# Performance work log

Hardware: AMD Instinct MI355X
Metric: run time of the kernel (lower is better)

Reference implementation:

```python
import jax, jax.numpy as jnp
import numpy as np

E = 512   # decoder embedding dim
H = 2048  # decoder hidden size


def setup_inputs() -> dict:
    key = jax.random.key(0)
    ks = jax.random.split(key, 10)
    V, B, T, S = 50000, 32, 128, 128
    s = 0.05
    return {
        "embed_table": jax.random.normal(ks[0], (V, E), jnp.float32) * s,
        "encoder_outs": jax.random.normal(ks[1], (S, B, 2 * 512), jnp.float32),
        "encoder_hiddens": jax.random.normal(ks[2], (1, B, H), jnp.float32) * s,
        "encoder_cells": jax.random.normal(ks[3], (1, B, H), jnp.float32) * s,
        "W_ih": jax.random.normal(ks[4], (4 * H, 2048), jnp.float32) * s,
        "W_hh": jax.random.normal(ks[5], (4 * H, H), jnp.float32) * s,
        "b_ih": jax.random.normal(ks[6], (4 * H,), jnp.float32) * s,
        "b_hh": jax.random.normal(ks[7], (4 * H,), jnp.float32) * s,
        "prev_output_tokens": jax.random.randint(ks[8], (B, T), 0, V),
        "tgt_langs": jax.random.randint(ks[9], (B,), 0, V),
    }


def reference(embed_table, encoder_outs, encoder_hiddens, encoder_cells,
              W_ih, W_hh, b_ih, b_hh, prev_output_tokens, tgt_langs):
    # bottleneck: max-pool encoder states over source time (LASER-style)
    context = jnp.max(encoder_outs, axis=0)                 # [B, 2*enc_hidden]
    x = embed_table[prev_output_tokens]                      # [B, T, E]
    x = jnp.transpose(x, (1, 0, 2))                          # [T, B, E]
    lang_embed = embed_table[tgt_langs]                      # [B, E]

    # Per-step LSTM input is concat(x_t, lang, context). lang/context are
    # time-invariant, so precompute their gate contribution once.
    static_in = jnp.concatenate([lang_embed, context], axis=1)   # [B, E + 2*enc]
    gates_x = (jnp.einsum('tbe,ge->tbg', x, W_ih[:, :E])
               + static_in @ W_ih[:, E:].T + b_ih + b_hh)        # [T, B, 4H]

    h0 = encoder_hiddens[0]
    c0 = encoder_cells[0]

    def step(carry, g_x):
        h, c = carry
        gates = g_x + h @ W_hh.T                              # [B, 4H]
        i, f, g, o = jnp.split(gates, 4, axis=1)
        c = jax.nn.sigmoid(f) * c + jax.nn.sigmoid(i) * jnp.tanh(g)
        h = jax.nn.sigmoid(o) * jnp.tanh(c)
        return (h, c), h

    _, outs = jax.lax.scan(step, (h0, c0), gates_x)           # [T, B, H]
    return outs
```

## Files before the change

### kernel.cpp

```cpp
#include <hip/hip_runtime.h>
#include <math.h>

#define E_DIM 512
#define H_DIM 2048
#define G_DIM 8192
#define B_DIM 32
#define T_DIM 128
#define S_DIM 128
#define ENC2  1024
#define SI_DIM 1536

#define NBLK 256
#define NTHR 512
#define JT   8
#define KHW  (H_DIM/8)
#define KXW  (E_DIM/8)
#define HB   (B_DIM*H_DIM)
#define HPLANE 65536



typedef __bf16 bf16_t;
typedef bf16_t bf16x8 __attribute__((ext_vector_type(8)));
typedef float f32x4 __attribute__((ext_vector_type(4)));
typedef unsigned int u32x4 __attribute__((ext_vector_type(4)));

__device__ __forceinline__ unsigned short f2bf(float x) {
    unsigned u = __float_as_uint(x);
    u += 0x7FFFu + ((u >> 16) & 1u);
    return (unsigned short)(u >> 16);
}
__device__ __forceinline__ float bf2f(unsigned short s) {
    return __uint_as_float(((unsigned)s) << 16);
}
__device__ __forceinline__ unsigned pack2(float a, float b) {
    return (unsigned)f2bf(a) | ((unsigned)f2bf(b) << 16);
}
__device__ __forceinline__ f32x4 mfma16(bf16x8 a, bf16x8 b, f32x4 c) {
    return __builtin_amdgcn_mfma_f32_16x16x32_bf16(a, b, c, 0, 0, 0);
}
__device__ __forceinline__ bf16x8 tofrag(u32x4 q) {
    return __builtin_bit_cast(bf16x8, q);
}
__device__ __forceinline__ float sigf(float x) { return 1.f / (1.f + expf(-x)); }

#define OPAQUE(v) asm volatile("" : "+v"(v))
#define ALD(p) __hip_atomic_load((p), __ATOMIC_RELAXED, __HIP_MEMORY_SCOPE_AGENT)
#define AST(p, v) __hip_atomic_store((p), (v), __ATOMIC_RELAXED, __HIP_MEMORY_SCOPE_AGENT)

struct WPair { u32x4 hi, lo; };
__device__ __forceinline__ WPair packW(const float* src) {
    float4 w0 = *(const float4*)src;
    float4 w1 = *(const float4*)(src + 16);
    u32x4 qh;
    qh.x = pack2(w0.x, w0.y); qh.y = pack2(w0.z, w0.w);
    qh.z = pack2(w1.x, w1.y); qh.w = pack2(w1.z, w1.w);
    float r0 = w0.x - bf2f((unsigned short)(qh.x & 0xFFFF));
    float r1 = w0.y - bf2f((unsigned short)(qh.x >> 16));
    float r2 = w0.z - bf2f((unsigned short)(qh.y & 0xFFFF));
    float r3 = w0.w - bf2f((unsigned short)(qh.y >> 16));
    float r4 = w1.x - bf2f((unsigned short)(qh.z & 0xFFFF));
    float r5 = w1.y - bf2f((unsigned short)(qh.z >> 16));
    float r6 = w1.z - bf2f((unsigned short)(qh.w & 0xFFFF));
    float r7 = w1.w - bf2f((unsigned short)(qh.w >> 16));
    u32x4 ql;
    ql.x = pack2(r0, r1); ql.y = pack2(r2, r3);
    ql.z = pack2(r4, r5); ql.w = pack2(r6, r7);
    WPair out; out.hi = qh; out.lo = ql;
    return out;
}

__global__ void k_prep(const float* __restrict__ enc_outs, const float* __restrict__ embed,
                       const int* __restrict__ langs, const float* __restrict__ h0,
                       float* __restrict__ si, unsigned short* __restrict__ hth,
                       unsigned short* __restrict__ htl, unsigned int* __restrict__ flags) {
    int tid = blockIdx.x * blockDim.x + threadIdx.x;
    int np = gridDim.x * blockDim.x;
    for (int i = tid; i < NBLK * 16; i += np)
        flags[i] = 0u;
    for (int i = tid; i < B_DIM * ENC2; i += np) {
        int b = i >> 10, e = i & 1023;
        float m = -3.4e38f;
        for (int s = 0; s < S_DIM; ++s)
            m = fmaxf(m, enc_outs[(s * B_DIM + b) * ENC2 + e]);
        si[b * SI_DIM + E_DIM + e] = m;
    }
    for (int i = tid; i < B_DIM * E_DIM; i += np) {
        int b = i >> 9, e = i & 511;
        si[b * SI_DIM + e] = embed[(long)langs[b] * E_DIM + e];
    }
    for (int i = tid; i < B_DIM * H_DIM; i += np) {
        int b = i >> 11, j = i & 2047;
        float h = h0[i];
        unsigned short hi = f2bf(h);
        unsigned short lo = f2bf(h - bf2f(hi));
        int T = j >> 5, lgp = (j & 15) >> 2, o = (j & 3) + 4 * ((j & 31) >> 4);
        int idx = ((T * 4 + lgp) * 32 + b) * 8 + o;
        hth[idx] = hi;
        htl[idx] = lo;
    }
}

__global__ void k_gather_x(const float* __restrict__ embed, const int* __restrict__ tok,
                           unsigned short* __restrict__ xh, unsigned short* __restrict__ xl) {
    int r = blockIdx.x;
    int t = r >> 5, b = r & 31;
    long row = tok[b * T_DIM + t];
    const float4* src = (const float4*)(embed + row * E_DIM);
    unsigned* xhp = (unsigned*)(xh + (size_t)t * 16384);
    unsigned* xlp = (unsigned*)(xl + (size_t)t * 16384);
    for (int g = threadIdx.x; g < 128; g += blockDim.x) {
        float4 v = src[g];
        unsigned h01 = pack2(v.x, v.y), h23 = pack2(v.z, v.w);
        float rx = v.x - bf2f((unsigned short)(h01 & 0xFFFF));
        float ry = v.y - bf2f((unsigned short)(h01 >> 16));
        float rz = v.z - bf2f((unsigned short)(h23 & 0xFFFF));
        float rw = v.w - bf2f((unsigned short)(h23 >> 16));
        int T = g >> 3, lgp = g & 3, o0 = 4 * ((g & 7) >> 2);
        int u32i = ((T * 4 + lgp) * 32 + b) * 4 + (o0 >> 1);
        uint2 qh; qh.x = h01; qh.y = h23;
        uint2 ql; ql.x = pack2(rx, ry); ql.y = pack2(rz, rw);
        *(uint2*)(xhp + u32i) = qh;
        *(uint2*)(xlp + u32i) = ql;
    }
}

#define MFMA12(PH, PL, IT) \
    acc00 = mfma16(Ah0, tofrag(PH##0##IT), acc00); \
    acc00 = mfma16(Ah0, tofrag(PL##0##IT), acc00); \
    acc00 = mfma16(Al0, tofrag(PH##0##IT), acc00); \
    acc01 = mfma16(Ah1, tofrag(PH##0##IT), acc01); \
    acc01 = mfma16(Ah1, tofrag(PL##0##IT), acc01); \
    acc01 = mfma16(Al1, tofrag(PH##0##IT), acc01); \
    acc10 = mfma16(Ah0, tofrag(PH##1##IT), acc10); \
    acc10 = mfma16(Ah0, tofrag(PL##1##IT), acc10); \
    acc10 = mfma16(Al0, tofrag(PH##1##IT), acc10); \
    acc11 = mfma16(Ah1, tofrag(PH##1##IT), acc11); \
    acc11 = mfma16(Ah1, tofrag(PL##1##IT), acc11); \
    acc11 = mfma16(Al1, tofrag(PH##1##IT), acc11);

#define AX_IT(IT) do { \
    const int fb = ((wv * 2 + (IT)) * 4 + lg) * 32 + lr; \
    bf16x8 Ah0 = __builtin_bit_cast(bf16x8, xh4[fb]); \
    bf16x8 Ah1 = __builtin_bit_cast(bf16x8, xh4[fb + 16]); \
    bf16x8 Al0 = __builtin_bit_cast(bf16x8, xl4[fb]); \
    bf16x8 Al1 = __builtin_bit_cast(bf16x8, xl4[fb + 16]); \
    MFMA12(Xh, Xl, IT) \
} while (0)

#define AH_IT(IT) do { \
    const int fb = ((wv * 8 + (IT)) * 4 + lg) * 32 + lr; \
    bf16x8 Ah0 = __builtin_bit_cast(bf16x8, hh4[fb]); \
    bf16x8 Ah1 = __builtin_bit_cast(bf16x8, hh4[fb + 16]); \
    bf16x8 Al0 = __builtin_bit_cast(bf16x8, hl4[fb]); \
    bf16x8 Al1 = __builtin_bit_cast(bf16x8, hl4[fb + 16]); \
    MFMA12(Wh, Wl, IT) \
} while (0)

#define PK_HH(F, IT) { WPair p = packW(W_hh + (long)rowf##F * H_DIM + (wv * KHW + IT * 32 + 4 * lg)); \
                       Wh##F##IT = p.hi; Wl##F##IT = p.lo; }
#define PK_X(F, IT)  { WPair p = packW(W_ih + (long)rowf##F * 2048 + (wv * KXW + IT * 32 + 4 * lg)); \
                       Xh##F##IT = p.hi; Xl##F##IT = p.lo; }

__global__ __launch_bounds__(NTHR, 2) void k_lstm(
        const unsigned short* __restrict__ xh, const unsigned short* __restrict__ xl,
        unsigned short* __restrict__ hth, unsigned short* __restrict__ htl,
        const float* __restrict__ si, const float* __restrict__ W_ih,
        const float* __restrict__ W_hh, const float* __restrict__ b_ih,
        const float* __restrict__ b_hh, const float* __restrict__ c0,
        float* __restrict__ out, unsigned int* __restrict__ flags) {
    __shared__ f32x4 red[8][2][2][64];
    __shared__ float sgl[4][B_DIM][JT];

    const int tid = threadIdx.x;
    const int wv = tid >> 6, l = tid & 63, lr = l & 15, lg = l >> 4;
    const int jb = blockIdx.x * JT;

    {
        int c = tid >> 4, bp = tid & 15;
        int gate = c >> 3, jl = c & 7;
        long grow = (long)(gate * H_DIM + jb + jl);
        const float* wrow = W_ih + grow * 2048 + E_DIM;
        const float* s0 = si + bp * SI_DIM;
        const float* s1 = si + (bp + 16) * SI_DIM;
        float a0 = 0.f, a1 = 0.f;
        for (int k = 0; k < SI_DIM; k += 4) {
            float4 w  = *(const float4*)(wrow + k);
            float4 x0 = *(const float4*)(s0 + k);
            float4 x1 = *(const float4*)(s1 + k);
            a0 += w.x * x0.x + w.y * x0.y + w.z * x0.z + w.w * x0.w;
            a1 += w.x * x1.x + w.y * x1.y + w.z * x1.z + w.w * x1.w;
        }
        float bias = b_ih[grow] + b_hh[grow];
        sgl[gate][bp][jl] = a0 + bias;
        sgl[gate][bp + 16][jl] = a1 + bias;
    }

    const int rowf0 = ((lr >> 3)) * H_DIM + jb + (lr & 7);
    const int rowf1 = (2 + (lr >> 3)) * H_DIM + jb + (lr & 7);

    u32x4 Wh00, Wh01, Wh02, Wh03, Wh04, Wh05, Wh06, Wh07;
    u32x4 Wh10, Wh11, Wh12, Wh13, Wh14, Wh15, Wh16, Wh17;
    u32x4 Wl00, Wl01, Wl02, Wl03, Wl04, Wl05, Wl06, Wl07;
    u32x4 Wl10, Wl11, Wl12, Wl13, Wl14, Wl15, Wl16, Wl17;
    u32x4 Xh00, Xh01, Xh10, Xh11, Xl00, Xl01, Xl10, Xl11;

    PK_HH(0, 0) PK_HH(0, 1) PK_HH(0, 2) PK_HH(0, 3)
    PK_HH(0, 4) PK_HH(0, 5) PK_HH(0, 6) PK_HH(0, 7)
    PK_HH(1, 0) PK_HH(1, 1) PK_HH(1, 2) PK_HH(1, 3)
    PK_HH(1, 4) PK_HH(1, 5) PK_HH(1, 6) PK_HH(1, 7)
    PK_X(0, 0) PK_X(0, 1) PK_X(1, 0) PK_X(1, 1)

    OPAQUE(Wh00); OPAQUE(Wh01); OPAQUE(Wh02); OPAQUE(Wh03);
    OPAQUE(Wh04); OPAQUE(Wh05); OPAQUE(Wh06); OPAQUE(Wh07);
    OPAQUE(Wh10); OPAQUE(Wh11); OPAQUE(Wh12); OPAQUE(Wh13);
    OPAQUE(Wh14); OPAQUE(Wh15); OPAQUE(Wh16); OPAQUE(Wh17);
    OPAQUE(Wl00); OPAQUE(Wl01); OPAQUE(Wl02); OPAQUE(Wl03);
    OPAQUE(Wl04); OPAQUE(Wl05); OPAQUE(Wl06); OPAQUE(Wl07);
    OPAQUE(Wl10); OPAQUE(Wl11); OPAQUE(Wl12); OPAQUE(Wl13);
    OPAQUE(Wl14); OPAQUE(Wl15); OPAQUE(Wl16); OPAQUE(Wl17);
    OPAQUE(Xh00); OPAQUE(Xh01); OPAQUE(Xh10); OPAQUE(Xh11);
    OPAQUE(Xl00); OPAQUE(Xl01); OPAQUE(Xl10); OPAQUE(Xl11);

    const int ab = tid >> 3, ajl = tid & 7;
    float creg = 0.f;
    if (tid < 256) creg = c0[ab * H_DIM + jb + ajl];

    __syncthreads();

    #pragma unroll 1
    for (int t = 0; t < T_DIM; ++t) {
        f32x4 acc00 = {}, acc01 = {}, acc10 = {}, acc11 = {};

        {
            const uint4* xh4 = (const uint4*)(xh + (size_t)t * 16384);
            const uint4* xl4 = (const uint4*)(xl + (size_t)t * 16384);
            AX_IT(0); AX_IT(1);
        }

        if (t > 0) {
            const unsigned tgt = (unsigned)t;
            const bool mine = (l < 32);
            const unsigned int* fp = flags + (size_t)(wv * 32 + (l & 31)) * 16;
            for (;;) {
                unsigned v = mine ? ALD(fp) : tgt;
                if (__all(v >= tgt)) break;
                __builtin_amdgcn_s_sleep(1);
            }
            __builtin_amdgcn_sched_barrier(0);
        }

        {
            const uint4* hh4 = (const uint4*)(hth + (size_t)t * HPLANE);
            const uint4* hl4 = (const uint4*)(htl + (size_t)t * HPLANE);
            AH_IT(0); AH_IT(1); AH_IT(2); AH_IT(3);
            AH_IT(4); AH_IT(5); AH_IT(6); AH_IT(7);
        }

        red[wv][0][0][l] = acc00; red[wv][0][1][l] = acc01;
        red[wv][1][0][l] = acc10; red[wv][1][1][l] = acc11;
        __syncthreads();

        float hn = 0.f;
        if (tid < 256) {
            const int m = ab >> 4, r = ab & 3, q = (ab & 15) >> 2;
            float gs[4];
            #pragma unroll
            for (int g = 0; g < 4; ++g) {
                const int l2 = (q << 4) | ((g & 1) * 8 + ajl);
                float s = 0.f;
                #pragma unroll
                for (int w = 0; w < 8; ++w)
                    s += red[w][g >> 1][m][l2][r];
                gs[g] = s + sgl[g][ab][ajl];
            }
            float cn = sigf(gs[1]) * creg + sigf(gs[0]) * tanhf(gs[2]);
            hn = sigf(gs[3]) * tanhf(cn);
            creg = cn;
            unsigned short hh = f2bf(hn);
            unsigned short hl = f2bf(hn - bf2f(hh));
            unsigned nhh = __shfl_down((unsigned)hh, 1);
            unsigned nhl = __shfl_down((unsigned)hl, 1);
            if ((ajl & 1) == 0) {
                unsigned* hthn = (unsigned*)(hth + (size_t)(t + 1) * HPLANE);
                unsigned* htln = (unsigned*)(htl + (size_t)(t + 1) * HPLANE);
                int j0 = jb + ajl;
                int T = j0 >> 5, lgp = (j0 & 15) >> 2;
                int o = (j0 & 3) + 4 * ((j0 & 31) >> 4);
                int u32i = ((T * 4 + lgp) * 32 + ab) * 4 + (o >> 1);
                AST(hthn + u32i, (unsigned)hh | (nhh << 16));
                AST(htln + u32i, (unsigned)hl | (nhl << 16));
            }
        }

        asm volatile("s_waitcnt vmcnt(0)" ::: "memory");
        __syncthreads();
        if (tid == 0 && t < T_DIM - 1)
            AST(flags + (size_t)blockIdx.x * 16, (unsigned)(t + 1));

        if (tid < 256)
            out[(size_t)t * HB + ab * H_DIM + jb + ajl] = hn;
    }
}

extern "C" void kernel_launch(void* const* d_in, const int* in_sizes, int n_in,
                              void* d_out, int out_size, void* d_ws, size_t ws_size,
                              hipStream_t stream) {
    const float* embed    = (const float*)d_in[0];
    const float* enc_outs = (const float*)d_in[1];
    const float* h0       = (const float*)d_in[2];
    const float* c0       = (const float*)d_in[3];
    const float* W_ih     = (const float*)d_in[4];
    const float* W_hh     = (const float*)d_in[5];
    const float* b_ih     = (const float*)d_in[6];
    const float* b_hh     = (const float*)d_in[7];
    const int*   tok      = (const int*)d_in[8];
    const int*   langs    = (const int*)d_in[9];
    float* out = (float*)d_out;

    char* ws = (char*)d_ws;
    unsigned short* xh  = (unsigned short*)(ws + 0);
    unsigned short* xl  = (unsigned short*)(ws + 4194304);
    unsigned short* hth = (unsigned short*)(ws + 8388608);
    unsigned short* htl = (unsigned short*)(ws + 25296896);
    float*          si  = (float*)(ws + 42205184);
    unsigned int* flags = (unsigned int*)(ws + 42401792);

    hipLaunchKernelGGL(k_prep, dim3(512), dim3(256), 0, stream,
                       enc_outs, embed, langs, h0, si, hth, htl, flags);
    hipLaunchKernelGGL(k_gather_x, dim3(T_DIM * B_DIM), dim3(128), 0, stream,
                       embed, tok, xh, xl);
    hipLaunchKernelGGL(k_lstm, dim3(NBLK), dim3(NTHR), 0, stream,
                       xh, xl, hth, htl, si, W_ih, W_hh, b_ih, b_hh, c0,
                       out, flags);
}
```

Measured before the change: 981.4 us.

## Split LSTM step into two batch-half phases with separate sync flags

Each timestep is now processed as two half-batch phases (batches 0-15 then 16-31). Each phase has its own grid-wide flag slot, so one half's recurrent matmul can proceed while other blocks are still finishing the other half. The aim is to let the inter-block barrier latency of one half overlap with compute on the other half. In exchange there are twice as many barriers and flag waits per step, smaller MFMA batches per phase, and fewer active threads in the elementwise stage.

```diff
diff --git a/kernel.cpp b/kernel.cpp
--- a/kernel.cpp
+++ b/kernel.cpp
@@ -125,42 +125,97 @@
     }
 }
 
-#define MFMA12(PH, PL, IT) \
-    acc00 = mfma16(Ah0, tofrag(PH##0##IT), acc00); \
-    acc00 = mfma16(Ah0, tofrag(PL##0##IT), acc00); \
-    acc00 = mfma16(Al0, tofrag(PH##0##IT), acc00); \
-    acc01 = mfma16(Ah1, tofrag(PH##0##IT), acc01); \
-    acc01 = mfma16(Ah1, tofrag(PL##0##IT), acc01); \
-    acc01 = mfma16(Al1, tofrag(PH##0##IT), acc01); \
-    acc10 = mfma16(Ah0, tofrag(PH##1##IT), acc10); \
-    acc10 = mfma16(Ah0, tofrag(PL##1##IT), acc10); \
-    acc10 = mfma16(Al0, tofrag(PH##1##IT), acc10); \
-    acc11 = mfma16(Ah1, tofrag(PH##1##IT), acc11); \
-    acc11 = mfma16(Ah1, tofrag(PL##1##IT), acc11); \
-    acc11 = mfma16(Al1, tofrag(PH##1##IT), acc11);
-
-#define AX_IT(IT) do { \
-    const int fb = ((wv * 2 + (IT)) * 4 + lg) * 32 + lr; \
-    bf16x8 Ah0 = __builtin_bit_cast(bf16x8, xh4[fb]); \
-    bf16x8 Ah1 = __builtin_bit_cast(bf16x8, xh4[fb + 16]); \
-    bf16x8 Al0 = __builtin_bit_cast(bf16x8, xl4[fb]); \
-    bf16x8 Al1 = __builtin_bit_cast(bf16x8, xl4[fb + 16]); \
-    MFMA12(Xh, Xl, IT) \
+#define MFMA6(PH, PL, IT) \
+    acc0 = mfma16(Ah, tofrag(PH##0##IT), acc0); \
+    acc0 = mfma16(Ah, tofrag(PL##0##IT), acc0); \
+    acc0 = mfma16(Al, tofrag(PH##0##IT), acc0); \
+    acc1 = mfma16(Ah, tofrag(PH##1##IT), acc1); \
+    acc1 = mfma16(Ah, tofrag(PL##1##IT), acc1); \
+    acc1 = mfma16(Al, tofrag(PH##1##IT), acc1);
+
+#define AX_IT(IT, BOFF) do { \
+    const int fb = ((wv * 2 + (IT)) * 4 + lg) * 32 + lr + (BOFF); \
+    bf16x8 Ah = __builtin_bit_cast(bf16x8, xh4[fb]); \
+    bf16x8 Al = __builtin_bit_cast(bf16x8, xl4[fb]); \
+    MFMA6(Xh, Xl, IT) \
 } while (0)
 
-#define AH_IT(IT) do { \
-    const int fb = ((wv * 8 + (IT)) * 4 + lg) * 32 + lr; \
-    bf16x8 Ah0 = __builtin_bit_cast(bf16x8, hh4[fb]); \
-    bf16x8 Ah1 = __builtin_bit_cast(bf16x8, hh4[fb + 16]); \
-    bf16x8 Al0 = __builtin_bit_cast(bf16x8, hl4[fb]); \
-    bf16x8 Al1 = __builtin_bit_cast(bf16x8, hl4[fb + 16]); \
-    MFMA12(Wh, Wl, IT) \
+#define AH_IT(IT, BOFF) do { \
+    const int fb = ((wv * 8 + (IT)) * 4 + lg) * 32 + lr + (BOFF); \
+    bf16x8 Ah = __builtin_bit_cast(bf16x8, hh4[fb]); \
+    bf16x8 Al = __builtin_bit_cast(bf16x8, hl4[fb]); \
+    MFMA6(Wh, Wl, IT) \
 } while (0)
 
 #define PK_HH(F, IT) { WPair p = packW(W_hh + (long)rowf##F * H_DIM + (wv * KHW + IT * 32 + 4 * lg)); \
                        Wh##F##IT = p.hi; Wl##F##IT = p.lo; }
 #define PK_X(F, IT)  { WPair p = packW(W_ih + (long)rowf##F * 2048 + (wv * KXW + IT * 32 + 4 * lg)); \
                        Xh##F##IT = p.hi; Xl##F##IT = p.lo; }
+
+#define HALF_PHASE(BOFF, SLOT, CREG) do { \
+    f32x4 acc0 = {}, acc1 = {}; \
+    { \
+        const uint4* xh4 = (const uint4*)(xh + (size_t)t * 16384); \
+        const uint4* xl4 = (const uint4*)(xl + (size_t)t * 16384); \
+        AX_IT(0, BOFF); AX_IT(1, BOFF); \
+    } \
+    if (t > 0) { \
+        const unsigned tgt = (unsigned)t; \
+        const bool mine = (l < 32); \
+        const unsigned int* fp = flags + (size_t)(wv * 32 + (l & 31)) * 16 + (SLOT); \
+        for (;;) { \
+            unsigned v = mine ? ALD(fp) : tgt; \
+            if (__all(v >= tgt)) break; \
+            __builtin_amdgcn_s_sleep(1); \
+        } \
+        __builtin_amdgcn_sched_barrier(0); \
+    } \
+    { \
+        const uint4* hh4 = (const uint4*)(hth + (size_t)t * HPLANE); \
+        const uint4* hl4 = (const uint4*)(htl + (size_t)t * HPLANE); \
+        AH_IT(0, BOFF); AH_IT(1, BOFF); AH_IT(2, BOFF); AH_IT(3, BOFF); \
+        AH_IT(4, BOFF); AH_IT(5, BOFF); AH_IT(6, BOFF); AH_IT(7, BOFF); \
+    } \
+    red[wv][0][l] = acc0; red[wv][1][l] = acc1; \
+    __syncthreads(); \
+    float hn = 0.f; \
+    if (tid < 128) { \
+        const int bh = tid >> 3, jl = tid & 7; \
+        const int r_ = bh & 3, q_ = bh >> 2; \
+        float gs[4]; \
+        _Pragma("unroll") \
+        for (int g = 0; g < 4; ++g) { \
+            const int l2 = (q_ << 4) | ((g & 1) * 8 + jl); \
+            float s = 0.f; \
+            _Pragma("unroll") \
+            for (int w = 0; w < 8; ++w) s += red[w][g >> 1][l2][r_]; \
+            gs[g] = s + sgl[g][(BOFF) + bh][jl]; \
+        } \
+        float cn = sigf(gs[1]) * (CREG) + sigf(gs[0]) * tanhf(gs[2]); \
+        hn = sigf(gs[3]) * tanhf(cn); \
+        (CREG) = cn; \
+        unsigned short hh_ = f2bf(hn); \
+        unsigned short hl_ = f2bf(hn - bf2f(hh_)); \
+        unsigned nhh = __shfl_down((unsigned)hh_, 1); \
+        unsigned nhl = __shfl_down((unsigned)hl_, 1); \
+        if ((jl & 1) == 0) { \
+            unsigned* hthn = (unsigned*)(hth + (size_t)(t + 1) * HPLANE); \
+            unsigned* htln = (unsigned*)(htl + (size_t)(t + 1) * HPLANE); \
+            const int j0 = jb + jl; \
+            const int Tt = j0 >> 5, lgp = (j0 & 15) >> 2; \
+            const int o_ = (j0 & 3) + 4 * ((j0 & 31) >> 4); \
+            const int u32i = ((Tt * 4 + lgp) * 32 + (BOFF) + bh) * 4 + (o_ >> 1); \
+            AST(hthn + u32i, (unsigned)hh_ | (nhh << 16)); \
+            AST(htln + u32i, (unsigned)hl_ | (nhl << 16)); \
+        } \
+    } \
+    asm volatile("s_waitcnt vmcnt(0)" ::: "memory"); \
+    __syncthreads(); \
+    if (tid == 0 && t < T_DIM - 1) \
+        AST(flags + (size_t)blockIdx.x * 16 + (SLOT), (unsigned)(t + 1)); \
+    if (tid < 128) \
+        out[(size_t)t * HB + ((BOFF) + (tid >> 3)) * H_DIM + jb + (tid & 7)] = hn; \
+} while (0)
 
 __global__ __launch_bounds__(NTHR, 2) void k_lstm(
         const unsigned short* __restrict__ xh, const unsigned short* __restrict__ xl,
@@ -169,7 +224,7 @@
         const float* __restrict__ W_hh, const float* __restrict__ b_ih,
         const float* __restrict__ b_hh, const float* __restrict__ c0,
         float* __restrict__ out, unsigned int* __restrict__ flags) {
-    __shared__ f32x4 red[8][2][2][64];
+    __shared__ f32x4 red[8][2][64];
     __shared__ float sgl[4][B_DIM][JT];
 
     const int tid = threadIdx.x;
@@ -222,84 +277,19 @@
     OPAQUE(Xh00); OPAQUE(Xh01); OPAQUE(Xh10); OPAQUE(Xh11);
     OPAQUE(Xl00); OPAQUE(Xl01); OPAQUE(Xl10); OPAQUE(Xl11);
 
-    const int ab = tid >> 3, ajl = tid & 7;
-    float creg = 0.f;
-    if (tid < 256) creg = c0[ab * H_DIM + jb + ajl];
+    float cregA = 0.f, cregB = 0.f;
+    if (tid < 128) {
+        const int bh = tid >> 3, jl = tid & 7;
+        cregA = c0[bh * H_DIM + jb + jl];
+        cregB = c0[(bh + 16) * H_DIM + jb + jl];
+    }
 
     __syncthreads();
 
     #pragma unroll 1
     for (int t = 0; t < T_DIM; ++t) {
-        f32x4 acc00 = {}, acc01 = {}, acc10 = {}, acc11 = {};
-
-        {
-            const uint4* xh4 = (const uint4*)(xh + (size_t)t * 16384);
-            const uint4* xl4 = (const uint4*)(xl + (size_t)t * 16384);
-            AX_IT(0); AX_IT(1);
-        }
-
-        if (t > 0) {
-            const unsigned tgt = (unsigned)t;
-            const bool mine = (l < 32);
-            const unsigned int* fp = flags + (size_t)(wv * 32 + (l & 31)) * 16;
-            for (;;) {
-                unsigned v = mine ? ALD(fp) : tgt;
-                if (__all(v >= tgt)) break;
-                __builtin_amdgcn_s_sleep(1);
-            }
-            __builtin_amdgcn_sched_barrier(0);
-        }
-
-        {
-            const uint4* hh4 = (const uint4*)(hth + (size_t)t * HPLANE);
-            const uint4* hl4 = (const uint4*)(htl + (size_t)t * HPLANE);
-            AH_IT(0); AH_IT(1); AH_IT(2); AH_IT(3);
-            AH_IT(4); AH_IT(5); AH_IT(6); AH_IT(7);
-        }
-
-        red[wv][0][0][l] = acc00; red[wv][0][1][l] = acc01;
-        red[wv][1][0][l] = acc10; red[wv][1][1][l] = acc11;
-        __syncthreads();
-
-        float hn = 0.f;
-        if (tid < 256) {
-            const int m = ab >> 4, r = ab & 3, q = (ab & 15) >> 2;
-            float gs[4];
-            #pragma unroll
-            for (int g = 0; g < 4; ++g) {
-                const int l2 = (q << 4) | ((g & 1) * 8 + ajl);
-                float s = 0.f;
-                #pragma unroll
-                for (int w = 0; w < 8; ++w)
-                    s += red[w][g >> 1][m][l2][r];
-                gs[g] = s + sgl[g][ab][ajl];
-            }
-            float cn = sigf(gs[1]) * creg + sigf(gs[0]) * tanhf(gs[2]);
-            hn = sigf(gs[3]) * tanhf(cn);
-            creg = cn;
-            unsigned short hh = f2bf(hn);
-            unsigned short hl = f2bf(hn - bf2f(hh));
-            unsigned nhh = __shfl_down((unsigned)hh, 1);
-            unsigned nhl = __shfl_down((unsigned)hl, 1);
-            if ((ajl & 1) == 0) {
-                unsigned* hthn = (unsigned*)(hth + (size_t)(t + 1) * HPLANE);
-                unsigned* htln = (unsigned*)(htl + (size_t)(t + 1) * HPLANE);
-                int j0 = jb + ajl;
-                int T = j0 >> 5, lgp = (j0 & 15) >> 2;
-                int o = (j0 & 3) + 4 * ((j0 & 31) >> 4);
-                int u32i = ((T * 4 + lgp) * 32 + ab) * 4 + (o >> 1);
-                AST(hthn + u32i, (unsigned)hh | (nhh << 16));
-                AST(htln + u32i, (unsigned)hl | (nhl << 16));
-            }
-        }
-
-        asm volatile("s_waitcnt vmcnt(0)" ::: "memory");
-        __syncthreads();
-        if (tid == 0 && t < T_DIM - 1)
-            AST(flags + (size_t)blockIdx.x * 16, (unsigned)(t + 1));
-
-        if (tid < 256)
-            out[(size_t)t * HB + ab * H_DIM + jb + ajl] = hn;
+        HALF_PHASE(0, 0, cregA);
+        HALF_PHASE(16, 1, cregB);
     }
 }
 
```

After: 1.311 ms. 1.34x slower.
